# Kernel optimization log

Hardware: AMD Instinct MI355X
Metric: run time of the kernel (lower is better)

Reference implementation:

```python
import jax, jax.numpy as jnp
import numpy as np

N = 50000   # nodes
E = 640000  # edges
H = 128     # input/hidden dim
C = 40      # classes
L = 2       # gnn layers


def _layernorm(h, g, b, eps=1e-5):
    mu = jnp.mean(h, axis=-1, keepdims=True)
    var = jnp.mean((h - mu) ** 2, axis=-1, keepdims=True)
    return (h - mu) * jax.lax.rsqrt(var + eps) * g + b


def setup_inputs() -> dict:
    key = jax.random.key(0)
    ks = jax.random.split(key, 20)
    s = 0.02
    inp = {
        "x": jax.random.normal(ks[0], (N, H), dtype=jnp.float32),
        "edge_index": jax.random.randint(ks[1], (2, E), 0, N, dtype=jnp.int64),
        # input projection MLP (Linear->ReLU->Dropout(eval)->Linear)
        "proj_w1": jax.random.normal(ks[2], (H, H), dtype=jnp.float32) * s,
        "proj_b1": jnp.zeros((H,), jnp.float32),
        "proj_w2": jax.random.normal(ks[3], (H, H), dtype=jnp.float32) * s,
        "proj_b2": jnp.zeros((H,), jnp.float32),
        "in_norm_g": jnp.ones((H,), jnp.float32),
        "in_norm_b": jnp.zeros((H,), jnp.float32),
        # stacked SAGEConv params: lin_l (on mean-aggregated neighbors, with bias),
        # lin_r (root weight, no bias) -- PyG SAGEConv defaults
        "sage_wl": jax.random.normal(ks[4], (L, H, H), dtype=jnp.float32) * s,
        "sage_bl": jnp.zeros((L, H), jnp.float32),
        "sage_wr": jax.random.normal(ks[5], (L, H, H), dtype=jnp.float32) * s,
        "ln_g": jnp.ones((L, H), jnp.float32),
        "ln_b": jnp.zeros((L, H), jnp.float32),
        # classifier MLP
        "cls_w1": jax.random.normal(ks[6], (H, H), dtype=jnp.float32) * s,
        "cls_b1": jnp.zeros((H,), jnp.float32),
        "cls_w2": jax.random.normal(ks[7], (H, C), dtype=jnp.float32) * s,
        "cls_b2": jnp.zeros((C,), jnp.float32),
    }
    return inp


def reference(x, edge_index, proj_w1, proj_b1, proj_w2, proj_b2,
              in_norm_g, in_norm_b, sage_wl, sage_bl, sage_wr,
              ln_g, ln_b, cls_w1, cls_b1, cls_w2, cls_b2):
    src = edge_index[0]  # message sources x_j
    dst = edge_index[1]  # aggregation targets
    # in-degree counts for mean aggregation (isolated nodes -> 0 output)
    cnt = jax.ops.segment_sum(jnp.ones((E,), jnp.float32), dst, num_segments=N)
    inv_cnt = jnp.where(cnt > 0, 1.0 / jnp.maximum(cnt, 1.0), 0.0)[:, None]

    # input projection + norm (dropout is identity in eval mode)
    h = jax.nn.relu(x @ proj_w1 + proj_b1) @ proj_w2 + proj_b2
    h = _layernorm(h, in_norm_g, in_norm_b)

    for l in range(L):
        msg_sum = jax.ops.segment_sum(h[src], dst, num_segments=N)  # [N,H]
        agg = msg_sum * inv_cnt  # mean aggregation
        h_next = agg @ sage_wl[l] + sage_bl[l] + h @ sage_wr[l]  # SAGEConv
        h_next = jax.nn.relu(h_next)
        h = _layernorm(h + h_next, ln_g[l], ln_b[l])  # residual + LayerNorm

    logits = jax.nn.relu(h @ cls_w1 + cls_b1) @ cls_w2 + cls_b2
    return (logits, h)
```

## Files before the change

### kernel.cpp

```cpp
#include <hip/hip_runtime.h>


namespace {

constexpr int NN = 50000;
constexpr int EE = 640000;
constexpr int HH = 128;
constexpr int CC = 40;
constexpr int SCAN_NB = (NN + 255) / 256;
constexpr int MG = (NN + 127) / 128;
constexpr int DEGB = (EE + 255) / 256;
constexpr int WPB = (5 * 16384 + CC * 128 + 255) / 256;
constexpr int FILLB = (EE + 255) / 256;

typedef unsigned short u16;
typedef __attribute__((ext_vector_type(8))) short s16x8;
typedef __attribute__((ext_vector_type(8))) unsigned short u16x8;
typedef __attribute__((ext_vector_type(4))) float f32x4;
typedef __attribute__((ext_vector_type(2))) float f32x2;

__device__ __forceinline__ float b2f(u16 h) {
  unsigned int u = ((unsigned int)h) << 16;
  return __builtin_bit_cast(float, u);
}
__device__ __forceinline__ u16 f2b(float f) {
  unsigned int u = __builtin_bit_cast(unsigned int, f);
  u += 0x7FFFu + ((u >> 16) & 1u);
  return (u16)(u >> 16);
}

__device__ __forceinline__ uint2 pack_fp8(const float* v) {
  int w0 = 0, w1 = 0;
  w0 = __builtin_amdgcn_cvt_pk_fp8_f32(v[0], v[1], w0, false);
  w0 = __builtin_amdgcn_cvt_pk_fp8_f32(v[2], v[3], w0, true);
  w1 = __builtin_amdgcn_cvt_pk_fp8_f32(v[4], v[5], w1, false);
  w1 = __builtin_amdgcn_cvt_pk_fp8_f32(v[6], v[7], w1, true);
  return make_uint2((unsigned)w0, (unsigned)w1);
}
__device__ __forceinline__ void acc_fp8(float* a, uint2 p) {
  const f32x2 f0 = __builtin_amdgcn_cvt_pk_f32_fp8((int)p.x, false);
  const f32x2 f1 = __builtin_amdgcn_cvt_pk_f32_fp8((int)p.x, true);
  const f32x2 f2 = __builtin_amdgcn_cvt_pk_f32_fp8((int)p.y, false);
  const f32x2 f3 = __builtin_amdgcn_cvt_pk_f32_fp8((int)p.y, true);
  a[0] += f0.x; a[1] += f0.y; a[2] += f1.x; a[3] += f1.y;
  a[4] += f2.x; a[5] += f2.y; a[6] += f3.x; a[7] += f3.y;
}

__device__ __forceinline__ s16x8 ldsw(const u16* base, int n, int k0) {
  return *reinterpret_cast<const s16x8*>(base + n * 128 + (((k0 ^ n) & 15) << 3));
}
__device__ __forceinline__ void stsw(u16* base, int r, int c, u16 v) {
  base[r * 128 + ((((c >> 3) ^ r) & 15) << 3) + (c & 7)] = v;
}
template <int NGRAN>
__device__ __forceinline__ void stage(const u16* __restrict__ src, u16* dst, int tid) {
#pragma unroll
  for (int i = 0; i < (NGRAN + 255) / 256; ++i) {
    const int gi = i * 256 + tid;
    if ((NGRAN & 255) == 0 || gi < NGRAN) {
      const int n = gi >> 4, k0 = gi & 15;
      const u16x8 v = *reinterpret_cast<const u16x8*>(src + gi * 8);
      *reinterpret_cast<u16x8*>(dst + n * 128 + (((k0 ^ n) & 15) << 3)) = v;
    }
  }
}

__global__ void k_pre(const float* __restrict__ pw1, const float* __restrict__ pw2,
                      u16* __restrict__ wt, int* __restrict__ cnt) {
  int flat = blockIdx.x * 256 + threadIdx.x;
  const int TWO = 2 * 16384;
  if (flat < TWO) {
    int id = flat >> 14;
    int off = flat & 16383;
    int n = off >> 7, k = off & 127;
    const float* s = id == 0 ? pw1 : pw2;
    wt[(size_t)id * 16384 + n * 128 + k] = f2b(s[k * 128 + n]);
  } else {
    int i = flat - TWO;
    if (i < NN) cnt[i] = 0;
  }
}

__global__ void k_scan_block(const int* __restrict__ cnt, int* __restrict__ rloc,
                             int* __restrict__ bsum, float* __restrict__ inv) {
  __shared__ int s[256];
  const int t = threadIdx.x;
  const int i = blockIdx.x * 256 + t;
  const int v = i < NN ? cnt[i] : 0;
  s[t] = v;
  __syncthreads();
  for (int off = 1; off < 256; off <<= 1) {
    int add = t >= off ? s[t - off] : 0;
    __syncthreads();
    s[t] += add;
    __syncthreads();
  }
  if (i < NN) {
    rloc[i] = s[t] - v;
    inv[i] = v > 0 ? 1.0f / (float)v : 0.0f;
  }
  if (t == 255) bsum[blockIdx.x] = s[255];
}

__global__ void k_scanfill(const int* __restrict__ rloc, const int* __restrict__ bsum,
                           int* __restrict__ rpf,
                           const int* __restrict__ ei, const int* __restrict__ rank,
                           u16* __restrict__ col) {
  __shared__ int s[256];
  const int t = threadIdx.x;
  {
    const int v = t < SCAN_NB ? bsum[t] : 0;
    s[t] = v;
    __syncthreads();
    for (int off = 1; off < 256; off <<= 1) {
      int add = t >= off ? s[t - off] : 0;
      __syncthreads();
      s[t] += add;
      __syncthreads();
    }
  }
  if (blockIdx.x < SCAN_NB) {
    const int boff = blockIdx.x == 0 ? 0 : s[blockIdx.x - 1];
    const int i = blockIdx.x * 256 + t;
    if (i < NN) rpf[i] = rloc[i] + boff;
    if (i == 0) rpf[NN] = EE;
  } else {
    const int e = (blockIdx.x - SCAN_NB) * 256 + t;
    if (e < EE) {
      const int d = ei[EE + e];
      const int bd = d >> 8;
      const int boff = bd == 0 ? 0 : s[bd - 1];
      col[rloc[d] + boff + rank[e]] = (u16)ei[e];
    }
  }
}

__global__ __launch_bounds__(256) void k_gather8(
    const unsigned char* __restrict__ h8, const int* __restrict__ rowptr,
    const u16* __restrict__ col, const float* __restrict__ inv,
    u16* __restrict__ agg) {
  const int tid = threadIdx.x;
  const int node = blockIdx.x * 16 + (tid >> 4);
  if (node >= NN) return;
  const int ln = tid & 15;
  const int cl = ln * 8;
  const int start = rowptr[node];
  const int end = rowptr[node + 1];
  float a[8] = {0.f, 0.f, 0.f, 0.f, 0.f, 0.f, 0.f, 0.f};
  int i = start;
  for (; i + 8 <= end; i += 8) {
    const int s0 = col[i], s1 = col[i + 1], s2 = col[i + 2], s3 = col[i + 3];
    const int s4 = col[i + 4], s5 = col[i + 5], s6 = col[i + 6], s7 = col[i + 7];
    const uint2 p0 = *reinterpret_cast<const uint2*>(&h8[(size_t)s0 * 128 + cl]);
    const uint2 p1 = *reinterpret_cast<const uint2*>(&h8[(size_t)s1 * 128 + cl]);
    const uint2 p2 = *reinterpret_cast<const uint2*>(&h8[(size_t)s2 * 128 + cl]);
    const uint2 p3 = *reinterpret_cast<const uint2*>(&h8[(size_t)s3 * 128 + cl]);
    const uint2 p4 = *reinterpret_cast<const uint2*>(&h8[(size_t)s4 * 128 + cl]);
    const uint2 p5 = *reinterpret_cast<const uint2*>(&h8[(size_t)s5 * 128 + cl]);
    const uint2 p6 = *reinterpret_cast<const uint2*>(&h8[(size_t)s6 * 128 + cl]);
    const uint2 p7 = *reinterpret_cast<const uint2*>(&h8[(size_t)s7 * 128 + cl]);
    acc_fp8(a, p0); acc_fp8(a, p1); acc_fp8(a, p2); acc_fp8(a, p3);
    acc_fp8(a, p4); acc_fp8(a, p5); acc_fp8(a, p6); acc_fp8(a, p7);
  }
  if (i + 4 <= end) {
    const int s0 = col[i], s1 = col[i + 1], s2 = col[i + 2], s3 = col[i + 3];
    const uint2 p0 = *reinterpret_cast<const uint2*>(&h8[(size_t)s0 * 128 + cl]);
    const uint2 p1 = *reinterpret_cast<const uint2*>(&h8[(size_t)s1 * 128 + cl]);
    const uint2 p2 = *reinterpret_cast<const uint2*>(&h8[(size_t)s2 * 128 + cl]);
    const uint2 p3 = *reinterpret_cast<const uint2*>(&h8[(size_t)s3 * 128 + cl]);
    acc_fp8(a, p0); acc_fp8(a, p1); acc_fp8(a, p2); acc_fp8(a, p3);
    i += 4;
  }
  for (; i < end; ++i) {
    const uint2 p0 = *reinterpret_cast<const uint2*>(&h8[(size_t)col[i] * 128 + cl]);
    acc_fp8(a, p0);
  }
  const float sc = inv[node];
#pragma unroll
  for (int k = 0; k < 8; ++k)
    agg[(size_t)node * 128 + k * 16 + ln] = f2b(a[k] * sc);
}

__global__ __launch_bounds__(256) void k_mlp_deg(
    const float* __restrict__ x, const u16* __restrict__ WT1,
    const float* __restrict__ pb1, const u16* __restrict__ WT2,
    const float* __restrict__ pb2, const float* __restrict__ lg,
    const float* __restrict__ lb, u16* __restrict__ hb,
    unsigned char* __restrict__ h8,
    const int* __restrict__ ei, int* __restrict__ cnt, int* __restrict__ rank,
    const float* __restrict__ swl, const float* __restrict__ swr,
    const float* __restrict__ cw1, const float* __restrict__ cw2,
    u16* __restrict__ wt) {
  __shared__ u16 lds[32768];
  if (blockIdx.x >= MG) {
    const int rb = blockIdx.x - MG;
    if (rb < DEGB) {
      const int e = rb * 256 + threadIdx.x;
      if (e < EE) rank[e] = atomicAdd(&cnt[ei[EE + e]], 1);
    } else {
      const int flat = (rb - DEGB) * 256 + threadIdx.x;
      const int FIVE = 5 * 16384;
      if (flat < FIVE) {
        int id = flat >> 14;
        int off = flat & 16383;
        int n = off >> 7, k = off & 127;
        const float* s;
        switch (id) {
          case 0: s = swl; break;
          case 1: s = swl + 16384; break;
          case 2: s = swr; break;
          case 3: s = swr + 16384; break;
          default: s = cw1; break;
        }
        wt[(size_t)(id + 2) * 16384 + n * 128 + k] = f2b(s[k * 128 + n]);
      } else {
        int off = flat - FIVE;
        if (off < CC * 128) {
          int n = off >> 7, k = off & 127;
          wt[(size_t)7 * 16384 + n * 128 + k] = f2b(cw2[k * CC + n]);
        }
      }
    }
    return;
  }
  u16* wreg = lds;
  u16* t1r = lds + 16384;
  const int tid = threadIdx.x;
  const int wv = tid >> 6, ln = tid & 63;
  const int lrow = ln & 15, kg = ln >> 4;
  const int tbase = blockIdx.x * 128 + wv * 32;
  const int lb0 = wv * 32;
  const int ar0 = min(tbase + lrow, NN - 1);
  const int ar1 = min(tbase + 16 + lrow, NN - 1);

  stage<2048>(WT1, wreg, tid);
  __syncthreads();

  f32x4 acc0[8], acc1[8];
#pragma unroll
  for (int cf = 0; cf < 8; ++cf) {
    acc0[cf] = (f32x4){0.f, 0.f, 0.f, 0.f};
    acc1[cf] = (f32x4){0.f, 0.f, 0.f, 0.f};
  }
#pragma unroll
  for (int ks = 0; ks < 4; ++ks) {
    const float4* p0 = reinterpret_cast<const float4*>(x + (size_t)ar0 * 128 + ks * 32 + kg * 8);
    const float4* p1 = reinterpret_cast<const float4*>(x + (size_t)ar1 * 128 + ks * 32 + kg * 8);
    float4 x0 = p0[0], x1 = p0[1], y0 = p1[0], y1 = p1[1];
    s16x8 a0, a1;
    a0[0] = (short)f2b(x0.x); a0[1] = (short)f2b(x0.y); a0[2] = (short)f2b(x0.z); a0[3] = (short)f2b(x0.w);
    a0[4] = (short)f2b(x1.x); a0[5] = (short)f2b(x1.y); a0[6] = (short)f2b(x1.z); a0[7] = (short)f2b(x1.w);
    a1[0] = (short)f2b(y0.x); a1[1] = (short)f2b(y0.y); a1[2] = (short)f2b(y0.z); a1[3] = (short)f2b(y0.w);
    a1[4] = (short)f2b(y1.x); a1[5] = (short)f2b(y1.y); a1[6] = (short)f2b(y1.z); a1[7] = (short)f2b(y1.w);
#pragma unroll
    for (int cf = 0; cf < 8; ++cf) {
      const s16x8 bf = ldsw(wreg, cf * 16 + lrow, ks * 4 + kg);
      acc0[cf] = __builtin_amdgcn_mfma_f32_16x16x32_bf16(a0, bf, acc0[cf], 0, 0, 0);
      acc1[cf] = __builtin_amdgcn_mfma_f32_16x16x32_bf16(a1, bf, acc1[cf], 0, 0, 0);
    }
  }
  {
    float bb[8];
#pragma unroll
    for (int cf = 0; cf < 8; ++cf) bb[cf] = pb1[cf * 16 + lrow];
#pragma unroll
    for (int t = 0; t < 2; ++t)
#pragma unroll
      for (int j = 0; j < 4; ++j) {
        const int lr = lb0 + t * 16 + kg * 4 + j;
#pragma unroll
        for (int cf = 0; cf < 8; ++cf)
          stsw(t1r, lr, cf * 16 + lrow, f2b(fmaxf((t ? acc1[cf][j] : acc0[cf][j]) + bb[cf], 0.0f)));
      }
  }
  __syncthreads();
  stage<2048>(WT2, wreg, tid);
  __syncthreads();

  f32x4 c0[8], c1[8];
#pragma unroll
  for (int cf = 0; cf < 8; ++cf) {
    c0[cf] = (f32x4){0.f, 0.f, 0.f, 0.f};
    c1[cf] = (f32x4){0.f, 0.f, 0.f, 0.f};
  }
#pragma unroll
  for (int ks = 0; ks < 4; ++ks) {
    const s16x8 a0 = ldsw(t1r, lb0 + lrow, ks * 4 + kg);
    const s16x8 a1 = ldsw(t1r, lb0 + 16 + lrow, ks * 4 + kg);
#pragma unroll
    for (int cf = 0; cf < 8; ++cf) {
      const s16x8 bf = ldsw(wreg, cf * 16 + lrow, ks * 4 + kg);
      c0[cf] = __builtin_amdgcn_mfma_f32_16x16x32_bf16(a0, bf, c0[cf], 0, 0, 0);
      c1[cf] = __builtin_amdgcn_mfma_f32_16x16x32_bf16(a1, bf, c1[cf], 0, 0, 0);
    }
  }

  float bb[8], gm[8], gb[8];
#pragma unroll
  for (int cf = 0; cf < 8; ++cf) {
    const int c = cf * 16 + lrow;
    bb[cf] = pb2[c];
    gm[cf] = lg[c];
    gb[cf] = lb[c];
  }
#pragma unroll
  for (int t = 0; t < 2; ++t)
#pragma unroll
    for (int j = 0; j < 4; ++j) {
      const int r = tbase + t * 16 + kg * 4 + j;
      float v[8];
#pragma unroll
      for (int cf = 0; cf < 8; ++cf) v[cf] = (t ? c1[cf][j] : c0[cf][j]) + bb[cf];
      float s = 0.f;
#pragma unroll
      for (int cf = 0; cf < 8; ++cf) s += v[cf];
      s += __shfl_xor(s, 1); s += __shfl_xor(s, 2);
      s += __shfl_xor(s, 4); s += __shfl_xor(s, 8);
      const float mu = s * (1.0f / 128);
      float q = 0.f;
#pragma unroll
      for (int cf = 0; cf < 8; ++cf) { const float d = v[cf] - mu; q += d * d; }
      q += __shfl_xor(q, 1); q += __shfl_xor(q, 2);
      q += __shfl_xor(q, 4); q += __shfl_xor(q, 8);
      const float istd = rsqrtf(q * (1.0f / 128) + 1e-5f);
      if (r < NN) {
        float ov[8];
#pragma unroll
        for (int cf = 0; cf < 8; ++cf) {
          ov[cf] = (v[cf] - mu) * istd * gm[cf] + gb[cf];
          hb[(size_t)r * 128 + cf * 16 + lrow] = f2b(ov[cf]);
        }
        *reinterpret_cast<uint2*>(&h8[(size_t)r * 128 + lrow * 8]) = pack_fp8(ov);
      }
    }
}

__global__ __launch_bounds__(256) void k_sage0(
    const u16* __restrict__ agg, const u16* __restrict__ hb,
    const u16* __restrict__ WTl, const u16* __restrict__ WTr,
    const float* __restrict__ bl, const float* __restrict__ lg,
    const float* __restrict__ lb, u16* __restrict__ hb_out,
    unsigned char* __restrict__ h8) {
  __shared__ u16 lds[32768];
  u16* wl = lds;
  u16* wr = lds + 16384;
  const int tid = threadIdx.x;
  const int wv = tid >> 6, ln = tid & 63;
  const int lrow = ln & 15, kg = ln >> 4;
  const int tbase = blockIdx.x * 128 + wv * 32;
  const int ar0 = min(tbase + lrow, NN - 1);
  const int ar1 = min(tbase + 16 + lrow, NN - 1);

  stage<2048>(WTl, wl, tid);
  stage<2048>(WTr, wr, tid);
  __syncthreads();

  f32x4 acc0[8], acc1[8];
#pragma unroll
  for (int cf = 0; cf < 8; ++cf) {
    acc0[cf] = (f32x4){0.f, 0.f, 0.f, 0.f};
    acc1[cf] = (f32x4){0.f, 0.f, 0.f, 0.f};
  }
#pragma unroll
  for (int ks = 0; ks < 4; ++ks) {
    const s16x8 g0 = *reinterpret_cast<const s16x8*>(agg + (size_t)ar0 * 128 + ks * 32 + kg * 8);
    const s16x8 g1 = *reinterpret_cast<const s16x8*>(agg + (size_t)ar1 * 128 + ks * 32 + kg * 8);
    const s16x8 h0 = *reinterpret_cast<const s16x8*>(hb + (size_t)ar0 * 128 + ks * 32 + kg * 8);
    const s16x8 h1 = *reinterpret_cast<const s16x8*>(hb + (size_t)ar1 * 128 + ks * 32 + kg * 8);
#pragma unroll
    for (int cf = 0; cf < 8; ++cf) {
      const s16x8 bwl = ldsw(wl, cf * 16 + lrow, ks * 4 + kg);
      const s16x8 bwr = ldsw(wr, cf * 16 + lrow, ks * 4 + kg);
      acc0[cf] = __builtin_amdgcn_mfma_f32_16x16x32_bf16(g0, bwl, acc0[cf], 0, 0, 0);
      acc0[cf] = __builtin_amdgcn_mfma_f32_16x16x32_bf16(h0, bwr, acc0[cf], 0, 0, 0);
      acc1[cf] = __builtin_amdgcn_mfma_f32_16x16x32_bf16(g1, bwl, acc1[cf], 0, 0, 0);
      acc1[cf] = __builtin_amdgcn_mfma_f32_16x16x32_bf16(h1, bwr, acc1[cf], 0, 0, 0);
    }
  }

  float bb[8], gm[8], gb[8];
#pragma unroll
  for (int cf = 0; cf < 8; ++cf) {
    const int c = cf * 16 + lrow;
    bb[cf] = bl[c];
    gm[cf] = lg[c];
    gb[cf] = lb[c];
  }
#pragma unroll
  for (int t = 0; t < 2; ++t)
#pragma unroll
    for (int j = 0; j < 4; ++j) {
      const int r = tbase + t * 16 + kg * 4 + j;
      const int rs = r < NN ? r : NN - 1;
      float v[8];
#pragma unroll
      for (int cf = 0; cf < 8; ++cf) {
        const int c = cf * 16 + lrow;
        v[cf] = b2f(hb[(size_t)rs * 128 + c]) +
                fmaxf((t ? acc1[cf][j] : acc0[cf][j]) + bb[cf], 0.0f);
      }
      float s = 0.f;
#pragma unroll
      for (int cf = 0; cf < 8; ++cf) s += v[cf];
      s += __shfl_xor(s, 1); s += __shfl_xor(s, 2);
      s += __shfl_xor(s, 4); s += __shfl_xor(s, 8);
      const float mu = s * (1.0f / 128);
      float q = 0.f;
#pragma unroll
      for (int cf = 0; cf < 8; ++cf) { const float d = v[cf] - mu; q += d * d; }
      q += __shfl_xor(q, 1); q += __shfl_xor(q, 2);
      q += __shfl_xor(q, 4); q += __shfl_xor(q, 8);
      const float istd = rsqrtf(q * (1.0f / 128) + 1e-5f);
      if (r < NN) {
        float ov[8];
#pragma unroll
        for (int cf = 0; cf < 8; ++cf) {
          ov[cf] = (v[cf] - mu) * istd * gm[cf] + gb[cf];
          hb_out[(size_t)r * 128 + cf * 16 + lrow] = f2b(ov[cf]);
        }
        *reinterpret_cast<uint2*>(&h8[(size_t)r * 128 + lrow * 8]) = pack_fp8(ov);
      }
    }
}

__global__ __launch_bounds__(256) void k_sage_cls(
    const u16* __restrict__ agg, const u16* __restrict__ hb,
    const u16* __restrict__ WTl, const u16* __restrict__ WTr,
    const float* __restrict__ bl, const float* __restrict__ lg,
    const float* __restrict__ lb,
    const u16* __restrict__ Wc1, const float* __restrict__ cb1,
    const u16* __restrict__ Wc2, const float* __restrict__ cb2,
    float* __restrict__ out_h, float* __restrict__ logits) {
  __shared__ u16 lds[37888];
  u16* wl = lds;
  u16* wr = lds + 16384;
  u16* w2 = lds + 32768;
  const int tid = threadIdx.x;
  const int wv = tid >> 6, ln = tid & 63;
  const int lrow = ln & 15, kg = ln >> 4;
  const int tbase = blockIdx.x * 128 + wv * 32;
  const int lb0 = wv * 32;
  const int ar0 = min(tbase + lrow, NN - 1);
  const int ar1 = min(tbase + 16 + lrow, NN - 1);

  stage<2048>(WTl, wl, tid);
  stage<2048>(WTr, wr, tid);
  stage<640>(Wc2, w2, tid);
  __syncthreads();

  f32x4 acc0[8], acc1[8];
#pragma unroll
  for (int cf = 0; cf < 8; ++cf) {
    acc0[cf] = (f32x4){0.f, 0.f, 0.f, 0.f};
    acc1[cf] = (f32x4){0.f, 0.f, 0.f, 0.f};
  }
#pragma unroll
  for (int ks = 0; ks < 4; ++ks) {
    const s16x8 g0 = *reinterpret_cast<const s16x8*>(agg + (size_t)ar0 * 128 + ks * 32 + kg * 8);
    const s16x8 g1 = *reinterpret_cast<const s16x8*>(agg + (size_t)ar1 * 128 + ks * 32 + kg * 8);
    const s16x8 h0 = *reinterpret_cast<const s16x8*>(hb + (size_t)ar0 * 128 + ks * 32 + kg * 8);
    const s16x8 h1 = *reinterpret_cast<const s16x8*>(hb + (size_t)ar1 * 128 + ks * 32 + kg * 8);
#pragma unroll
    for (int cf = 0; cf < 8; ++cf) {
      const s16x8 bwl = ldsw(wl, cf * 16 + lrow, ks * 4 + kg);
      const s16x8 bwr = ldsw(wr, cf * 16 + lrow, ks * 4 + kg);
      acc0[cf] = __builtin_amdgcn_mfma_f32_16x16x32_bf16(g0, bwl, acc0[cf], 0, 0, 0);
      acc0[cf] = __builtin_amdgcn_mfma_f32_16x16x32_bf16(h0, bwr, acc0[cf], 0, 0, 0);
      acc1[cf] = __builtin_amdgcn_mfma_f32_16x16x32_bf16(g1, bwl, acc1[cf], 0, 0, 0);
      acc1[cf] = __builtin_amdgcn_mfma_f32_16x16x32_bf16(h1, bwr, acc1[cf], 0, 0, 0);
    }
  }
  __syncthreads();

  {
    float bb[8], gm[8], gb[8];
#pragma unroll
    for (int cf = 0; cf < 8; ++cf) {
      const int c = cf * 16 + lrow;
      bb[cf] = bl[c];
      gm[cf] = lg[c];
      gb[cf] = lb[c];
    }
#pragma unroll
    for (int t = 0; t < 2; ++t)
#pragma unroll
      for (int j = 0; j < 4; ++j) {
        const int r = tbase + t * 16 + kg * 4 + j;
        const int rs = r < NN ? r : NN - 1;
        const int lr = lb0 + t * 16 + kg * 4 + j;
        float v[8];
#pragma unroll
        for (int cf = 0; cf < 8; ++cf) {
          const int c = cf * 16 + lrow;
          v[cf] = b2f(hb[(size_t)rs * 128 + c]) +
                  fmaxf((t ? acc1[cf][j] : acc0[cf][j]) + bb[cf], 0.0f);
        }
        float s = 0.f;
#pragma unroll
        for (int cf = 0; cf < 8; ++cf) s += v[cf];
        s += __shfl_xor(s, 1); s += __shfl_xor(s, 2);
        s += __shfl_xor(s, 4); s += __shfl_xor(s, 8);
        const float mu = s * (1.0f / 128);
        float q = 0.f;
#pragma unroll
        for (int cf = 0; cf < 8; ++cf) { const float d = v[cf] - mu; q += d * d; }
        q += __shfl_xor(q, 1); q += __shfl_xor(q, 2);
        q += __shfl_xor(q, 4); q += __shfl_xor(q, 8);
        const float istd = rsqrtf(q * (1.0f / 128) + 1e-5f);
#pragma unroll
        for (int cf = 0; cf < 8; ++cf) {
          const int c = cf * 16 + lrow;
          const float o = (v[cf] - mu) * istd * gm[cf] + gb[cf];
          stsw(wl, lr, c, f2b(o));
          if (r < NN) out_h[(size_t)r * 128 + c] = o;
        }
      }
  }
  stage<2048>(Wc1, wr, tid);
  __syncthreads();

  float cb1v[8];
#pragma unroll
  for (int cf = 0; cf < 8; ++cf) cb1v[cf] = cb1[cf * 16 + lrow];

#pragma unroll
  for (int t = 0; t < 2; ++t) {
    const int rb = lb0 + t * 16;
    f32x4 a3[8];
#pragma unroll
    for (int cf = 0; cf < 8; ++cf) a3[cf] = (f32x4){0.f, 0.f, 0.f, 0.f};
#pragma unroll
    for (int ks = 0; ks < 4; ++ks) {
      const s16x8 a = ldsw(wl, rb + lrow, ks * 4 + kg);
#pragma unroll
      for (int cf = 0; cf < 8; ++cf) {
        const s16x8 bf = ldsw(wr, cf * 16 + lrow, ks * 4 + kg);
        a3[cf] = __builtin_amdgcn_mfma_f32_16x16x32_bf16(a, bf, a3[cf], 0, 0, 0);
      }
    }
#pragma unroll
    for (int j = 0; j < 4; ++j)
#pragma unroll
      for (int cf = 0; cf < 8; ++cf)
        stsw(wl, rb + kg * 4 + j, cf * 16 + lrow, f2b(fmaxf(a3[cf][j] + cb1v[cf], 0.0f)));

    f32x4 a2[3];
#pragma unroll
    for (int cf = 0; cf < 3; ++cf) a2[cf] = (f32x4){0.f, 0.f, 0.f, 0.f};
#pragma unroll
    for (int ks = 0; ks < 4; ++ks) {
      const s16x8 a = ldsw(wl, rb + lrow, ks * 4 + kg);
#pragma unroll
      for (int cf = 0; cf < 3; ++cf) {
        const int bn = min(cf * 16 + lrow, CC - 1);
        const s16x8 bf = ldsw(w2, bn, ks * 4 + kg);
        a2[cf] = __builtin_amdgcn_mfma_f32_16x16x32_bf16(a, bf, a2[cf], 0, 0, 0);
      }
    }
#pragma unroll
    for (int j = 0; j < 4; ++j) {
      const int r = tbase + t * 16 + kg * 4 + j;
      if (r < NN) {
#pragma unroll
        for (int cf = 0; cf < 3; ++cf) {
          const int c = cf * 16 + lrow;
          if (c < CC) logits[(size_t)r * CC + c] = a2[cf][j] + cb2[c];
        }
      }
    }
  }
}

}

extern "C" void kernel_launch(void* const* d_in, const int* in_sizes, int n_in,
                              void* d_out, int out_size, void* d_ws, size_t ws_size,
                              hipStream_t stream) {
  (void)in_sizes; (void)n_in; (void)out_size; (void)ws_size;
  const float* x   = (const float*)d_in[0];
  const int*   ei  = (const int*)d_in[1];
  const float* pw1 = (const float*)d_in[2];
  const float* pb1 = (const float*)d_in[3];
  const float* pw2 = (const float*)d_in[4];
  const float* pb2 = (const float*)d_in[5];
  const float* ing = (const float*)d_in[6];
  const float* inb = (const float*)d_in[7];
  const float* swl = (const float*)d_in[8];
  const float* sbl = (const float*)d_in[9];
  const float* swr = (const float*)d_in[10];
  const float* lng = (const float*)d_in[11];
  const float* lnb = (const float*)d_in[12];
  const float* cw1 = (const float*)d_in[13];
  const float* cb1 = (const float*)d_in[14];
  const float* cw2 = (const float*)d_in[15];
  const float* cb2 = (const float*)d_in[16];

  float* out_logits = (float*)d_out;
  float* out_h = out_logits + (size_t)NN * CC;

  const size_t NNH = (size_t)NN * HH;
  u16*   hb   = (u16*)d_ws;
  u16*   bufA = hb + NNH;
  u16*   wt   = bufA + NNH;
  int*   cnt    = (int*)(wt + 8 * 16384);
  float* inv    = (float*)(cnt + NN);
  int*   rloc   = (int*)(inv + NN);
  int*   rpf    = rloc + NN;
  int*   bsum   = rpf + NN + 1;
  int*   rankar = bsum + 256;
  u16*   colarr = (u16*)(rankar + EE);
  unsigned char* h8 = (unsigned char*)(colarr + EE);

  const int PRE_B = (2 * 16384 + NN + 255) / 256;
  k_pre<<<PRE_B, 256, 0, stream>>>(pw1, pw2, wt, cnt);

  k_mlp_deg<<<MG + DEGB + WPB, 256, 0, stream>>>(
      x, wt + 0 * 16384, pb1, wt + 1 * 16384, pb2, ing, inb, hb, h8,
      ei, cnt, rankar, swl, swr, cw1, cw2, wt);

  k_scan_block<<<SCAN_NB, 256, 0, stream>>>(cnt, rloc, bsum, inv);
  k_scanfill<<<SCAN_NB + FILLB, 256, 0, stream>>>(rloc, bsum, rpf, ei, rankar, colarr);

  k_gather8<<<(NN + 15) / 16, 256, 0, stream>>>(h8, rpf, colarr, inv, bufA);
  k_sage0<<<(NN + 127) / 128, 256, 0, stream>>>(
      bufA, hb, wt + 2 * 16384, wt + 4 * 16384, sbl, lng, lnb, hb, h8);

  k_gather8<<<(NN + 15) / 16, 256, 0, stream>>>(h8, rpf, colarr, inv, bufA);
  k_sage_cls<<<(NN + 127) / 128, 256, 0, stream>>>(
      bufA, hb, wt + 3 * 16384, wt + 5 * 16384, sbl + HH, lng + HH, lnb + HH,
      wt + 6 * 16384, cb1, wt + 7 * 16384, cb2, out_h, out_logits);
}
```

Measured before the change: 140.1 us.

## Split degree counters into eight partitions to reduce atomic contention

```diff
diff --git a/kernel.cpp b/kernel.cpp
--- a/kernel.cpp
+++ b/kernel.cpp
@@ -66,7 +66,7 @@
 }
 
 __global__ void k_pre(const float* __restrict__ pw1, const float* __restrict__ pw2,
-                      u16* __restrict__ wt, int* __restrict__ cnt) {
+                      u16* __restrict__ wt, int* __restrict__ cnt8) {
   int flat = blockIdx.x * 256 + threadIdx.x;
   const int TWO = 2 * 16384;
   if (flat < TWO) {
@@ -77,16 +77,26 @@
     wt[(size_t)id * 16384 + n * 128 + k] = f2b(s[k * 128 + n]);
   } else {
     int i = flat - TWO;
-    if (i < NN) cnt[i] = 0;
-  }
-}
-
-__global__ void k_scan_block(const int* __restrict__ cnt, int* __restrict__ rloc,
-                             int* __restrict__ bsum, float* __restrict__ inv) {
+    if (i < 8 * NN) cnt8[i] = 0;
+  }
+}
+
+__global__ void k_scan_block(const int* __restrict__ cnt8, int* __restrict__ rloc,
+                             int* __restrict__ bsum, float* __restrict__ inv,
+                             u16* __restrict__ pcum) {
   __shared__ int s[256];
   const int t = threadIdx.x;
   const int i = blockIdx.x * 256 + t;
-  const int v = i < NN ? cnt[i] : 0;
+  int v = 0;
+  if (i < NN) {
+    int run = 0;
+#pragma unroll
+    for (int q = 0; q < 8; ++q) {
+      pcum[q * NN + i] = (u16)run;
+      run += cnt8[q * NN + i];
+    }
+    v = run;
+  }
   s[t] = v;
   __syncthreads();
   for (int off = 1; off < 256; off <<= 1) {
@@ -105,7 +115,7 @@
 __global__ void k_scanfill(const int* __restrict__ rloc, const int* __restrict__ bsum,
                            int* __restrict__ rpf,
                            const int* __restrict__ ei, const int* __restrict__ rank,
-                           u16* __restrict__ col) {
+                           const u16* __restrict__ pcum, u16* __restrict__ col) {
   __shared__ int s[256];
   const int t = threadIdx.x;
   {
@@ -130,7 +140,9 @@
       const int d = ei[EE + e];
       const int bd = d >> 8;
       const int boff = bd == 0 ? 0 : s[bd - 1];
-      col[rloc[d] + boff + rank[e]] = (u16)ei[e];
+      const int rk = rank[e];
+      const int p = rk & 7, rp = rk >> 3;
+      col[rloc[d] + boff + (int)pcum[p * NN + d] + rp] = (u16)ei[e];
     }
   }
 }
@@ -187,7 +199,7 @@
     const float* __restrict__ pb2, const float* __restrict__ lg,
     const float* __restrict__ lb, u16* __restrict__ hb,
     unsigned char* __restrict__ h8,
-    const int* __restrict__ ei, int* __restrict__ cnt, int* __restrict__ rank,
+    const int* __restrict__ ei, int* __restrict__ cnt8, int* __restrict__ rank,
     const float* __restrict__ swl, const float* __restrict__ swr,
     const float* __restrict__ cw1, const float* __restrict__ cw2,
     u16* __restrict__ wt) {
@@ -196,7 +208,12 @@
     const int rb = blockIdx.x - MG;
     if (rb < DEGB) {
       const int e = rb * 256 + threadIdx.x;
-      if (e < EE) rank[e] = atomicAdd(&cnt[ei[EE + e]], 1);
+      if (e < EE) {
+        const int p = blockIdx.x & 7;
+        const int d = ei[EE + e];
+        const int rp = atomicAdd(&cnt8[p * NN + d], 1);
+        rank[e] = (rp << 3) | p;
+      }
     } else {
       const int flat = (rb - DEGB) * 256 + threadIdx.x;
       const int FIVE = 5 * 16384;
@@ -602,24 +619,25 @@
   u16*   hb   = (u16*)d_ws;
   u16*   bufA = hb + NNH;
   u16*   wt   = bufA + NNH;
-  int*   cnt    = (int*)(wt + 8 * 16384);
-  float* inv    = (float*)(cnt + NN);
+  int*   cnt8   = (int*)(wt + 8 * 16384);
+  float* inv    = (float*)(cnt8 + 8 * NN);
   int*   rloc   = (int*)(inv + NN);
   int*   rpf    = rloc + NN;
   int*   bsum   = rpf + NN + 1;
-  int*   rankar = bsum + 256;
+  u16*   pcum   = (u16*)(bsum + 256);
+  int*   rankar = (int*)(pcum + 8 * NN);
   u16*   colarr = (u16*)(rankar + EE);
   unsigned char* h8 = (unsigned char*)(colarr + EE);
 
-  const int PRE_B = (2 * 16384 + NN + 255) / 256;
-  k_pre<<<PRE_B, 256, 0, stream>>>(pw1, pw2, wt, cnt);
+  const int PRE_B = (2 * 16384 + 8 * NN + 255) / 256;
+  k_pre<<<PRE_B, 256, 0, stream>>>(pw1, pw2, wt, cnt8);
 
   k_mlp_deg<<<MG + DEGB + WPB, 256, 0, stream>>>(
       x, wt + 0 * 16384, pb1, wt + 1 * 16384, pb2, ing, inb, hb, h8,
-      ei, cnt, rankar, swl, swr, cw1, cw2, wt);
-
-  k_scan_block<<<SCAN_NB, 256, 0, stream>>>(cnt, rloc, bsum, inv);
-  k_scanfill<<<SCAN_NB + FILLB, 256, 0, stream>>>(rloc, bsum, rpf, ei, rankar, colarr);
+      ei, cnt8, rankar, swl, swr, cw1, cw2, wt);
+
+  k_scan_block<<<SCAN_NB, 256, 0, stream>>>(cnt8, rloc, bsum, inv, pcum);
+  k_scanfill<<<SCAN_NB + FILLB, 256, 0, stream>>>(rloc, bsum, rpf, ei, rankar, pcum, colarr);
 
   k_gather8<<<(NN + 15) / 16, 256, 0, stream>>>(h8, rpf, colarr, inv, bufA);
   k_sage0<<<(NN + 127) / 128, 256, 0, stream>>>(
```

Result: slower. 143.6 us (+2.5%).
